# Optimization experiments

Measured on AMD Instinct MI355X. Metric: run time of the kernel, lower is better.

## Reference

```python
import jax, jax.numpy as jnp
import numpy as np

NUM_HEADS = 32
NUM_KV_HEADS = 8  # num_heads // 4 (GQA)
HEAD_DIM = 64     # hidden_size // num_heads
ROPE_BASE = 10000.0


def _rotate_half(x):
    x1, x2 = jnp.split(x, 2, axis=-1)
    return jnp.concatenate((-x2, x1), axis=-1)


def _rope_cos_sin(seq_len, dtype):
    inv_freq = 1.0 / (ROPE_BASE ** (jnp.arange(0, HEAD_DIM, 2, dtype=jnp.float32) / HEAD_DIM))
    t = jnp.arange(seq_len, dtype=jnp.float32)
    freqs = jnp.outer(t, inv_freq)                 # [S, HEAD_DIM//2]
    emb = jnp.concatenate((freqs, freqs), axis=-1) # [S, HEAD_DIM]
    return jnp.cos(emb).astype(dtype), jnp.sin(emb).astype(dtype)


def setup_inputs() -> dict:
    key = jax.random.key(0)
    ks = jax.random.split(key, 5)
    B, S, H = 1, 2048, 2048
    KV = NUM_KV_HEADS * HEAD_DIM  # 512
    s = 0.02
    return {
        "hidden_states": jax.random.normal(ks[0], (B, S, H), jnp.float32),
        "Wq": jax.random.normal(ks[1], (H, H), jnp.float32) * s,
        "Wk": jax.random.normal(ks[2], (KV, H), jnp.float32) * s,
        "Wv": jax.random.normal(ks[3], (KV, H), jnp.float32) * s,
        "Wo": jax.random.normal(ks[4], (H, H), jnp.float32) * s,
    }


def reference(hidden_states, Wq, Wk, Wv, Wo):
    B, S, H = hidden_states.shape
    dtype = hidden_states.dtype
    # QKV projections (nn.Linear with weight [out,in], no bias)
    q = jnp.einsum("bsh,oh->bso", hidden_states, Wq)
    k = jnp.einsum("bsh,oh->bso", hidden_states, Wk)
    v = jnp.einsum("bsh,oh->bso", hidden_states, Wv)
    q = q.reshape(B, S, NUM_HEADS, HEAD_DIM).transpose(0, 2, 1, 3)      # [B,H,S,D]
    k = k.reshape(B, S, NUM_KV_HEADS, HEAD_DIM).transpose(0, 2, 1, 3)   # [B,KV,S,D]
    v = v.reshape(B, S, NUM_KV_HEADS, HEAD_DIM).transpose(0, 2, 1, 3)
    # RoPE
    cos, sin = _rope_cos_sin(S, dtype)  # [S,D] broadcast over batch/heads
    q = q * cos + _rotate_half(q) * sin
    k = k * cos + _rotate_half(k) * sin
    # GQA: repeat_interleave KV heads
    groups = NUM_HEADS // NUM_KV_HEADS
    k = jnp.repeat(k, groups, axis=1)
    v = jnp.repeat(v, groups, axis=1)
    # Attention: scores in fp32 softmax, causal mask (additive)
    scale = 1.0 / np.sqrt(HEAD_DIM)
    scores = jnp.einsum("bhqd,bhkd->bhqk", q, k) * scale
    causal = jnp.tril(jnp.ones((S, S), dtype=bool))
    scores = jnp.where(causal, scores, jnp.finfo(jnp.float32).min)
    probs = jax.nn.softmax(scores.astype(jnp.float32), axis=-1).astype(dtype)
    attn = jnp.einsum("bhqk,bhkd->bhqd", probs, v)
    attn = attn.transpose(0, 2, 1, 3).reshape(B, S, H)
    return jnp.einsum("bsh,oh->bso", attn, Wo)
```

## Files before the change

kernel.cpp:

```cpp
#include <hip/hip_runtime.h>
#include <hip/hip_bf16.h>
#include <math.h>

typedef __hip_bfloat16 bf16;
typedef __attribute__((ext_vector_type(8))) short short8;
typedef __attribute__((ext_vector_type(4))) short short4v;
typedef __attribute__((ext_vector_type(4))) float floatx4;

#define MFMA16(a, b, c) __builtin_amdgcn_mfma_f32_16x16x32_bf16((a), (b), (c), 0, 0, 0)

typedef const __attribute__((address_space(1))) void* as1_cvp;
typedef __attribute__((address_space(3))) void* as3_vp;

__device__ __forceinline__ void gload_lds16(const bf16* g, bf16* lds_uni) {
    __builtin_amdgcn_global_load_lds((as1_cvp)g, (as3_vp)lds_uni, 16, 0, 0);
}

__global__ __launch_bounds__(256) void cvt_all(
    const float* __restrict__ a0, const float* __restrict__ a1,
    const float* __restrict__ a2, const float* __restrict__ a3,
    const float* __restrict__ a4,
    bf16* __restrict__ d0, bf16* __restrict__ d1, bf16* __restrict__ d2,
    bf16* __restrict__ d3, bf16* __restrict__ d4)
{
    const int b = blockIdx.x;
    const float* src; bf16* dst; int off;
    if (b < 2048)      { src = a0; dst = d0; off = b; }
    else if (b < 4096) { src = a1; dst = d1; off = b - 2048; }
    else if (b < 4608) { src = a2; dst = d2; off = b - 4096; }
    else if (b < 5120) { src = a3; dst = d3; off = b - 4608; }
    else               { src = a4; dst = d4; off = b - 5120; }
    const int i = (off * 256 + threadIdx.x) * 8;
    const float4 x = *(const float4*)(src + i);
    const float4 y = *(const float4*)(src + i + 4);
    bf16 t[8];
    t[0] = __float2bfloat16(x.x); t[1] = __float2bfloat16(x.y);
    t[2] = __float2bfloat16(x.z); t[3] = __float2bfloat16(x.w);
    t[4] = __float2bfloat16(y.x); t[5] = __float2bfloat16(y.y);
    t[6] = __float2bfloat16(y.z); t[7] = __float2bfloat16(y.w);
    *(short8*)(dst + i) = *(const short8*)t;
}

#define GEMM_K_LOOP_12864(KB)                                                   \
    for (int k0 = 0; k0 < (KB); k0 += 64) {                                     \
        gload_lds16(gA + k0,            ldsA);                                  \
        gload_lds16(gA + A64 + k0,      ldsA + 2048);                           \
        gload_lds16(gB + k0,            ldsB);                                  \
        gload_lds16(gA + k0 + 32,       ldsA + 4096);                           \
        gload_lds16(gA + A64 + k0 + 32, ldsA + 6144);                           \
        gload_lds16(gB + k0 + 32,       ldsB + 2048);                           \
        __syncthreads();                                                        \
        _Pragma("unroll")                                                       \
        for (int hh = 0; hh < 2; ++hh) {                                        \
            short8 af[2], bfr[4];                                               \
            _Pragma("unroll")                                                   \
            for (int i = 0; i < 2; ++i)                                         \
                af[i] = *(const short8*)&As[hh * 4096 + (w * 32 + i * 16 + l15) * 32 + quad * 8]; \
            _Pragma("unroll")                                                   \
            for (int j = 0; j < 4; ++j)                                         \
                bfr[j] = *(const short8*)&Bs[hh * 2048 + (j * 16 + l15) * 32 + quad * 8]; \
            _Pragma("unroll")                                                   \
            for (int i = 0; i < 2; ++i)                                         \
                _Pragma("unroll")                                               \
                for (int j = 0; j < 4; ++j)                                     \
                    acc[i][j] = MFMA16(af[i], bfr[j], acc[i][j]);               \
        }                                                                       \
        __syncthreads();                                                        \
    }

__global__ __launch_bounds__(256) void gemm_qkv(
    const bf16* __restrict__ A, const bf16* __restrict__ Wq,
    const bf16* __restrict__ Wk, const bf16* __restrict__ Wv,
    bf16* __restrict__ qb, bf16* __restrict__ kb, bf16* __restrict__ vt)
{
    constexpr int LDK = 2048;
    __shared__ bf16 As[2 * 128 * 32];
    __shared__ bf16 Bs[2 * 64 * 32];

    const int tid  = threadIdx.x;
    const int lane = tid & 63;
    const int w    = tid >> 6;
    const int quad = lane >> 4, l15 = lane & 15;
    const int bx = blockIdx.x, by = blockIdx.y;

    const bf16* Bp; int bxl, mode;
    if (bx < 32)      { Bp = Wq; bxl = bx;      mode = 0; }
    else if (bx < 40) { Bp = Wk; bxl = bx - 32; mode = 1; }
    else              { Bp = Wv; bxl = bx - 40; mode = 2; }

    floatx4 acc[2][4];
#pragma unroll
    for (int i = 0; i < 2; ++i)
#pragma unroll
        for (int j = 0; j < 4; ++j) {
            floatx4 z = {0.f, 0.f, 0.f, 0.f};
            acc[i][j] = z;
        }

    const int srow = tid >> 2;
    const int sch  = (tid & 3) * 8;
    const bf16* gA = A  + (size_t)(by * 128 + srow) * LDK + sch;
    const bf16* gB = Bp + (size_t)(bxl * 64 + srow) * LDK + sch;
    const size_t A64 = (size_t)64 * LDK;
    bf16* ldsA = As + w * 512;
    bf16* ldsB = Bs + w * 512;

    GEMM_K_LOOP_12864(LDK)

    if (mode == 2) {
#pragma unroll
        for (int i = 0; i < 2; ++i)
#pragma unroll
            for (int j = 0; j < 4; ++j) {
                const int col = bxl * 64 + j * 16 + l15;
                const int rowb = by * 128 + w * 32 + i * 16 + quad * 4;
                bf16 t[4];
#pragma unroll
                for (int r = 0; r < 4; ++r) t[r] = __float2bfloat16(acc[i][j][r]);
                *(short4v*)&vt[(size_t)col * 2048 + rowb] = *(const short4v*)t;
            }
    } else {
        bf16* C = (mode == 0) ? qb : kb;
        const int Nn = (mode == 0) ? 2048 : 512;
        const float scale = (mode == 0) ? 0.125f : 1.0f;
        const float LOG2_1E4 = 13.28771237954945f;
        const float ifr0 = exp2f(-((float)l15) * (LOG2_1E4 / 32.f));
        const float ifr1 = exp2f(-((float)(16 + l15)) * (LOG2_1E4 / 32.f));
#pragma unroll
        for (int i = 0; i < 2; ++i) {
#pragma unroll
            for (int r = 0; r < 4; ++r) {
                const int row = by * 128 + w * 32 + i * 16 + quad * 4 + r;
                float s0, c0, s1, c1;
                sincosf((float)row * ifr0, &s0, &c0);
                sincosf((float)row * ifr1, &s1, &c1);
#pragma unroll
                for (int j = 0; j < 4; ++j) {
                    const float x  = acc[i][j][r];
                    const float xp = acc[i][j ^ 2][r];
                    const float cs = (j & 1) ? c1 : c0;
                    const float sn = (j & 1) ? s1 : s0;
                    const float oo = (x * cs + ((j < 2) ? -xp : xp) * sn) * scale;
                    const int col = bxl * 64 + j * 16 + l15;
                    C[(size_t)row * Nn + col] = __float2bfloat16(oo);
                }
            }
        }
    }
}

__global__ __launch_bounds__(256) void gemm_out(
    const bf16* __restrict__ A, const bf16* __restrict__ B, float* __restrict__ C)
{
    constexpr int LDK = 2048;
    __shared__ bf16 As[2 * 128 * 32];
    __shared__ bf16 Bs[2 * 64 * 32];

    const int tid  = threadIdx.x;
    const int lane = tid & 63;
    const int w    = tid >> 6;
    const int quad = lane >> 4, l15 = lane & 15;
    const int bx = blockIdx.x, by = blockIdx.y;

    floatx4 acc[2][4];
#pragma unroll
    for (int i = 0; i < 2; ++i)
#pragma unroll
        for (int j = 0; j < 4; ++j) {
            floatx4 z = {0.f, 0.f, 0.f, 0.f};
            acc[i][j] = z;
        }

    const int srow = tid >> 2;
    const int sch  = (tid & 3) * 8;
    const bf16* gA = A + (size_t)(by * 128 + srow) * LDK + sch;
    const bf16* gB = B + (size_t)(bx * 64 + srow) * LDK + sch;
    const size_t A64 = (size_t)64 * LDK;
    bf16* ldsA = As + w * 512;
    bf16* ldsB = Bs + w * 512;

    GEMM_K_LOOP_12864(LDK)

#pragma unroll
    for (int i = 0; i < 2; ++i)
#pragma unroll
        for (int j = 0; j < 4; ++j)
#pragma unroll
            for (int r = 0; r < 4; ++r) {
                const int row = by * 128 + w * 32 + i * 16 + quad * 4 + r;
                const int col = bx * 64 + j * 16 + l15;
                C[(size_t)row * 2048 + col] = acc[i][j][r];
            }
}

__global__ __launch_bounds__(256) void fattn5(
    const bf16* __restrict__ q, const bf16* __restrict__ k,
    const bf16* __restrict__ vt, bf16* __restrict__ o)
{
    __shared__ bf16 Ks[2][64 * 72];
    __shared__ bf16 Vs[2][64 * 72];
    __shared__ bf16 Ps[4][16 * 68];

    const int a = 31 - blockIdx.x;
    const int h = blockIdx.y;
    const int kvh = h >> 2;
    const int tid = threadIdx.x, lane = tid & 63, w = tid >> 6;
    const int quad = lane >> 4, l15 = lane & 15;
    bf16* P = Ps[w];

    short ob[8];
#pragma unroll
    for (int e = 0; e < 8; ++e) ob[e] = (short)0x3F80;
    const short8 ones = *(const short8*)ob;

    const int srow = tid >> 3;
    const int ch8  = (tid & 7) * 8;
    const bf16* kg = k  + (size_t)kvh * 64 + ch8;
    const bf16* vg = vt + (size_t)(kvh * 64 + srow) * 2048 + ch8;

    const int qrow0 = a * 64 + w * 16;

    short8 qf[2];
#pragma unroll
    for (int ks = 0; ks < 2; ++ks)
        qf[ks] = *(const short8*)&q[(size_t)(qrow0 + l15) * 2048 + h * 64 + ks * 32 + quad * 8];

    floatx4 o_acc[4], l_acc;
#pragma unroll
    for (int n4 = 0; n4 < 4; ++n4) {
        floatx4 z = {0.f, 0.f, 0.f, 0.f};
        o_acc[n4] = z;
    }
    { floatx4 z = {0.f, 0.f, 0.f, 0.f}; l_acc = z; }

    {
        short8 k0 = *(const short8*)(kg + (size_t)srow * 512);
        short8 k1 = *(const short8*)(kg + (size_t)(srow + 32) * 512);
        short8 v0 = *(const short8*)(vg);
        short8 v1 = *(const short8*)(vg + (size_t)32 * 2048);
        *(short8*)&Ks[0][srow * 72 + ch8]        = k0;
        *(short8*)&Ks[0][(srow + 32) * 72 + ch8] = k1;
        *(short8*)&Vs[0][srow * 72 + ch8]        = v0;
        *(short8*)&Vs[0][(srow + 32) * 72 + ch8] = v1;
    }
    __syncthreads();

    for (int kt = 0; kt <= a; ++kt) {
        const int buf = kt & 1;

        short8 nk0, nk1, nv0, nv1;
        if (kt < a) {
            const size_t kr = (size_t)((kt + 1) * 64) * 512;
            nk0 = *(const short8*)(kg + kr + (size_t)srow * 512);
            nk1 = *(const short8*)(kg + kr + (size_t)(srow + 32) * 512);
            nv0 = *(const short8*)(vg + (kt + 1) * 64);
            nv1 = *(const short8*)(vg + (size_t)32 * 2048 + (kt + 1) * 64);
        }

        floatx4 s_acc[4];
#pragma unroll
        for (int n = 0; n < 4; ++n) {
            floatx4 z = {0.f, 0.f, 0.f, 0.f};
            s_acc[n] = z;
        }
        __builtin_amdgcn_s_setprio(1);
#pragma unroll
        for (int n = 0; n < 4; ++n)
#pragma unroll
            for (int ks = 0; ks < 2; ++ks) {
                const short8 kf = *(const short8*)&Ks[buf][(n * 16 + l15) * 72 + ks * 32 + quad * 8];
                s_acc[n] = MFMA16(kf, qf[ks], s_acc[n]);
            }
        __builtin_amdgcn_s_setprio(0);

        if (kt < a) {
#pragma unroll
            for (int n = 0; n < 4; ++n) {
                bf16 t4[4];
#pragma unroll
                for (int r = 0; r < 4; ++r)
                    t4[r] = __float2bfloat16(__expf(s_acc[n][r]));
                *(short4v*)&P[l15 * 68 + n * 16 + quad * 4] = *(const short4v*)t4;
            }
        } else {
#pragma unroll
            for (int n = 0; n < 4; ++n) {
                bf16 t4[4];
#pragma unroll
                for (int r = 0; r < 4; ++r) {
                    const bool okc = (n * 16 + quad * 4 + r) <= (w * 16 + l15);
                    t4[r] = __float2bfloat16(okc ? __expf(s_acc[n][r]) : 0.f);
                }
                *(short4v*)&P[l15 * 68 + n * 16 + quad * 4] = *(const short4v*)t4;
            }
        }

        __builtin_amdgcn_s_setprio(1);
#pragma unroll
        for (int ks2 = 0; ks2 < 2; ++ks2) {
            const short8 pf = *(const short8*)&P[l15 * 68 + ks2 * 32 + quad * 8];
            l_acc = MFMA16(pf, ones, l_acc);
#pragma unroll
            for (int n4 = 0; n4 < 4; ++n4) {
                const short8 vf = *(const short8*)&Vs[buf][(n4 * 16 + l15) * 72 + ks2 * 32 + quad * 8];
                o_acc[n4] = MFMA16(pf, vf, o_acc[n4]);
            }
        }
        __builtin_amdgcn_s_setprio(0);

        if (kt < a) {
            *(short8*)&Ks[buf ^ 1][srow * 72 + ch8]        = nk0;
            *(short8*)&Ks[buf ^ 1][(srow + 32) * 72 + ch8] = nk1;
            *(short8*)&Vs[buf ^ 1][srow * 72 + ch8]        = nv0;
            *(short8*)&Vs[buf ^ 1][(srow + 32) * 72 + ch8] = nv1;
        }
        __syncthreads();
    }

#pragma unroll
    for (int n4 = 0; n4 < 4; ++n4)
#pragma unroll
        for (int r = 0; r < 4; ++r) {
            const float val = o_acc[n4][r] / l_acc[r];
            const int row = qrow0 + quad * 4 + r;
            const int col = h * 64 + n4 * 16 + l15;
            o[(size_t)row * 2048 + col] = __float2bfloat16(val);
        }
}

extern "C" void kernel_launch(void* const* d_in, const int* in_sizes, int n_in,
                              void* d_out, int out_size, void* d_ws, size_t ws_size,
                              hipStream_t stream)
{
    const float* hs = (const float*)d_in[0];
    const float* Wq = (const float*)d_in[1];
    const float* Wk = (const float*)d_in[2];
    const float* Wv = (const float*)d_in[3];
    const float* Wo = (const float*)d_in[4];
    float* out = (float*)d_out;

    bf16* ws  = (bf16*)d_ws;
    bf16* hsb = ws;
    bf16* Wqb = ws + 4194304;
    bf16* Wkb = ws + 8388608;
    bf16* Wvb = ws + 9437184;
    bf16* Wob = ws + 10485760;
    bf16* qb  = ws + 14680064;
    bf16* kb  = ws + 18874368;
    bf16* vtb = ws + 19922944;
    bf16* ab  = ws + 20971520;

    dim3 blk(256);
    cvt_all<<<7168, blk, 0, stream>>>(hs, Wq, Wk, Wv, Wo, hsb, Wqb, Wkb, Wvb, Wob);
    gemm_qkv<<<dim3(48, 16), blk, 0, stream>>>(hsb, Wqb, Wkb, Wvb, qb, kb, vtb);
    fattn5<<<dim3(32, 32), blk, 0, stream>>>(qb, kb, vtb, ab);
    gemm_out<<<dim3(32, 16), blk, 0, stream>>>(ab, Wob, out);
}
```

Before: 262.5 us.

## Pair causal query tiles per block and load K/V directly into registers

```diff
diff --git a/kernel.cpp b/kernel.cpp
--- a/kernel.cpp
+++ b/kernel.cpp
@@ -193,16 +193,15 @@
             }
 }
 
-__global__ __launch_bounds__(256) void fattn5(
+__global__ __launch_bounds__(256) void fattn6(
     const bf16* __restrict__ q, const bf16* __restrict__ k,
     const bf16* __restrict__ vt, bf16* __restrict__ o)
 {
-    __shared__ bf16 Ks[2][64 * 72];
-    __shared__ bf16 Vs[2][64 * 72];
     __shared__ bf16 Ps[4][16 * 68];
 
-    const int a = 31 - blockIdx.x;
-    const int h = blockIdx.y;
+    const int id = blockIdx.x;
+    const int h = id & 31;
+    const int tpair = id >> 5;
     const int kvh = h >> 2;
     const int tid = threadIdx.x, lane = tid & 63, w = tid >> 6;
     const int quad = lane >> 4, l15 = lane & 15;
@@ -213,119 +212,119 @@
     for (int e = 0; e < 8; ++e) ob[e] = (short)0x3F80;
     const short8 ones = *(const short8*)ob;
 
-    const int srow = tid >> 3;
-    const int ch8  = (tid & 7) * 8;
-    const bf16* kg = k  + (size_t)kvh * 64 + ch8;
-    const bf16* vg = vt + (size_t)(kvh * 64 + srow) * 2048 + ch8;
-
-    const int qrow0 = a * 64 + w * 16;
-
-    short8 qf[2];
-#pragma unroll
-    for (int ks = 0; ks < 2; ++ks)
-        qf[ks] = *(const short8*)&q[(size_t)(qrow0 + l15) * 2048 + h * 64 + ks * 32 + quad * 8];
-
-    floatx4 o_acc[4], l_acc;
-#pragma unroll
-    for (int n4 = 0; n4 < 4; ++n4) {
-        floatx4 z = {0.f, 0.f, 0.f, 0.f};
-        o_acc[n4] = z;
+    const bf16* kgl = k  + (size_t)l15 * 512 + kvh * 64 + quad * 8;
+    const bf16* vgl = vt + (size_t)(kvh * 64 + l15) * 2048 + quad * 8;
+
+#pragma unroll 1
+    for (int ph = 0; ph < 2; ++ph) {
+        const int a = ph ? (31 - tpair) : tpair;
+        const int qrow0 = a * 64 + w * 16;
+
+        short8 qf[2];
+#pragma unroll
+        for (int ks = 0; ks < 2; ++ks)
+            qf[ks] = *(const short8*)&q[(size_t)(qrow0 + l15) * 2048 + h * 64 + ks * 32 + quad * 8];
+
+        floatx4 o_acc[4], l_acc;
+#pragma unroll
+        for (int n4 = 0; n4 < 4; ++n4) {
+            floatx4 z = {0.f, 0.f, 0.f, 0.f};
+            o_acc[n4] = z;
+        }
+        { floatx4 z = {0.f, 0.f, 0.f, 0.f}; l_acc = z; }
+
+        short8 kf[4][2];
+#pragma unroll
+        for (int n = 0; n < 4; ++n)
+#pragma unroll
+            for (int ks = 0; ks < 2; ++ks)
+                kf[n][ks] = *(const short8*)(kgl + (size_t)(n * 16) * 512 + ks * 32);
+
+        for (int kt = 0; kt <= a; ++kt) {
+            short8 vf[4][2];
+#pragma unroll
+            for (int n4 = 0; n4 < 4; ++n4)
+#pragma unroll
+                for (int ks2 = 0; ks2 < 2; ++ks2)
+                    vf[n4][ks2] = *(const short8*)(vgl + (size_t)(n4 * 16) * 2048
+                                                   + kt * 64 + ks2 * 32);
+
+            floatx4 s_acc[4];
+#pragma unroll
+            for (int n = 0; n < 4; ++n) {
+                floatx4 z = {0.f, 0.f, 0.f, 0.f};
+                s_acc[n] = z;
+            }
+            __builtin_amdgcn_s_setprio(1);
+#pragma unroll
+            for (int n = 0; n < 4; ++n)
+#pragma unroll
+                for (int ks = 0; ks < 2; ++ks)
+                    s_acc[n] = MFMA16(kf[n][ks], qf[ks], s_acc[n]);
+            __builtin_amdgcn_s_setprio(0);
+
+            short8 kn[4][2];
+            if (kt < a) {
+                const bf16* kgn = kgl + (size_t)((kt + 1) * 64) * 512;
+#pragma unroll
+                for (int n = 0; n < 4; ++n)
+#pragma unroll
+                    for (int ks = 0; ks < 2; ++ks)
+                        kn[n][ks] = *(const short8*)(kgn + (size_t)(n * 16) * 512 + ks * 32);
+            }
+
+            if (kt < a) {
+#pragma unroll
+                for (int n = 0; n < 4; ++n) {
+                    bf16 t4[4];
+#pragma unroll
+                    for (int r = 0; r < 4; ++r)
+                        t4[r] = __float2bfloat16(__expf(s_acc[n][r]));
+                    *(short4v*)&P[l15 * 68 + n * 16 + quad * 4] = *(const short4v*)t4;
+                }
+            } else {
+#pragma unroll
+                for (int n = 0; n < 4; ++n) {
+                    bf16 t4[4];
+#pragma unroll
+                    for (int r = 0; r < 4; ++r) {
+                        const bool okc = (n * 16 + quad * 4 + r) <= (w * 16 + l15);
+                        t4[r] = __float2bfloat16(okc ? __expf(s_acc[n][r]) : 0.f);
+                    }
+                    *(short4v*)&P[l15 * 68 + n * 16 + quad * 4] = *(const short4v*)t4;
+                }
+            }
+
+            __builtin_amdgcn_s_setprio(1);
+#pragma unroll
+            for (int ks2 = 0; ks2 < 2; ++ks2) {
+                const short8 pf = *(const short8*)&P[l15 * 68 + ks2 * 32 + quad * 8];
+                l_acc = MFMA16(pf, ones, l_acc);
+#pragma unroll
+                for (int n4 = 0; n4 < 4; ++n4)
+                    o_acc[n4] = MFMA16(pf, vf[n4][ks2], o_acc[n4]);
+            }
+            __builtin_amdgcn_s_setprio(0);
+
+            if (kt < a) {
+#pragma unroll
+                for (int n = 0; n < 4; ++n)
+#pragma unroll
+                    for (int ks = 0; ks < 2; ++ks)
+                        kf[n][ks] = kn[n][ks];
+            }
+        }
+
+#pragma unroll
+        for (int n4 = 0; n4 < 4; ++n4)
+#pragma unroll
+            for (int r = 0; r < 4; ++r) {
+                const float val = o_acc[n4][r] / l_acc[r];
+                const int row = qrow0 + quad * 4 + r;
+                const int col = h * 64 + n4 * 16 + l15;
+                o[(size_t)row * 2048 + col] = __float2bfloat16(val);
+            }
     }
-    { floatx4 z = {0.f, 0.f, 0.f, 0.f}; l_acc = z; }
-
-    {
-        short8 k0 = *(const short8*)(kg + (size_t)srow * 512);
-        short8 k1 = *(const short8*)(kg + (size_t)(srow + 32) * 512);
-        short8 v0 = *(const short8*)(vg);
-        short8 v1 = *(const short8*)(vg + (size_t)32 * 2048);
-        *(short8*)&Ks[0][srow * 72 + ch8]        = k0;
-        *(short8*)&Ks[0][(srow + 32) * 72 + ch8] = k1;
-        *(short8*)&Vs[0][srow * 72 + ch8]        = v0;
-        *(short8*)&Vs[0][(srow + 32) * 72 + ch8] = v1;
-    }
-    __syncthreads();
-
-    for (int kt = 0; kt <= a; ++kt) {
-        const int buf = kt & 1;
-
-        short8 nk0, nk1, nv0, nv1;
-        if (kt < a) {
-            const size_t kr = (size_t)((kt + 1) * 64) * 512;
-            nk0 = *(const short8*)(kg + kr + (size_t)srow * 512);
-            nk1 = *(const short8*)(kg + kr + (size_t)(srow + 32) * 512);
-            nv0 = *(const short8*)(vg + (kt + 1) * 64);
-            nv1 = *(const short8*)(vg + (size_t)32 * 2048 + (kt + 1) * 64);
-        }
-
-        floatx4 s_acc[4];
-#pragma unroll
-        for (int n = 0; n < 4; ++n) {
-            floatx4 z = {0.f, 0.f, 0.f, 0.f};
-            s_acc[n] = z;
-        }
-        __builtin_amdgcn_s_setprio(1);
-#pragma unroll
-        for (int n = 0; n < 4; ++n)
-#pragma unroll
-            for (int ks = 0; ks < 2; ++ks) {
-                const short8 kf = *(const short8*)&Ks[buf][(n * 16 + l15) * 72 + ks * 32 + quad * 8];
-                s_acc[n] = MFMA16(kf, qf[ks], s_acc[n]);
-            }
-        __builtin_amdgcn_s_setprio(0);
-
-        if (kt < a) {
-#pragma unroll
-            for (int n = 0; n < 4; ++n) {
-                bf16 t4[4];
-#pragma unroll
-                for (int r = 0; r < 4; ++r)
-                    t4[r] = __float2bfloat16(__expf(s_acc[n][r]));
-                *(short4v*)&P[l15 * 68 + n * 16 + quad * 4] = *(const short4v*)t4;
-            }
-        } else {
-#pragma unroll
-            for (int n = 0; n < 4; ++n) {
-                bf16 t4[4];
-#pragma unroll
-                for (int r = 0; r < 4; ++r) {
-                    const bool okc = (n * 16 + quad * 4 + r) <= (w * 16 + l15);
-                    t4[r] = __float2bfloat16(okc ? __expf(s_acc[n][r]) : 0.f);
-                }
-                *(short4v*)&P[l15 * 68 + n * 16 + quad * 4] = *(const short4v*)t4;
-            }
-        }
-
-        __builtin_amdgcn_s_setprio(1);
-#pragma unroll
-        for (int ks2 = 0; ks2 < 2; ++ks2) {
-            const short8 pf = *(const short8*)&P[l15 * 68 + ks2 * 32 + quad * 8];
-            l_acc = MFMA16(pf, ones, l_acc);
-#pragma unroll
-            for (int n4 = 0; n4 < 4; ++n4) {
-                const short8 vf = *(const short8*)&Vs[buf][(n4 * 16 + l15) * 72 + ks2 * 32 + quad * 8];
-                o_acc[n4] = MFMA16(pf, vf, o_acc[n4]);
-            }
-        }
-        __builtin_amdgcn_s_setprio(0);
-
-        if (kt < a) {
-            *(short8*)&Ks[buf ^ 1][srow * 72 + ch8]        = nk0;
-            *(short8*)&Ks[buf ^ 1][(srow + 32) * 72 + ch8] = nk1;
-            *(short8*)&Vs[buf ^ 1][srow * 72 + ch8]        = nv0;
-            *(short8*)&Vs[buf ^ 1][(srow + 32) * 72 + ch8] = nv1;
-        }
-        __syncthreads();
-    }
-
-#pragma unroll
-    for (int n4 = 0; n4 < 4; ++n4)
-#pragma unroll
-        for (int r = 0; r < 4; ++r) {
-            const float val = o_acc[n4][r] / l_acc[r];
-            const int row = qrow0 + quad * 4 + r;
-            const int col = h * 64 + n4 * 16 + l15;
-            o[(size_t)row * 2048 + col] = __float2bfloat16(val);
-        }
 }
 
 extern "C" void kernel_launch(void* const* d_in, const int* in_sizes, int n_in,
@@ -353,6 +352,6 @@
     dim3 blk(256);
     cvt_all<<<7168, blk, 0, stream>>>(hs, Wq, Wk, Wv, Wo, hsb, Wqb, Wkb, Wvb, Wob);
     gemm_qkv<<<dim3(48, 16), blk, 0, stream>>>(hsb, Wqb, Wkb, Wvb, qb, kb, vtb);
-    fattn5<<<dim3(32, 32), blk, 0, stream>>>(qb, kb, vtb, ab);
+    fattn6<<<dim3(512), blk, 0, stream>>>(qb, kb, vtb, ab);
     gemm_out<<<dim3(32, 16), blk, 0, stream>>>(ab, Wob, out);
 }
```

After: 290.4 us. 10.6% more time.
